# Optimization experiments

Hardware: AMD Instinct MI355X
Metric: run time of the kernel (lower is better)

Reference implementation:

```python
import jax, jax.numpy as jnp
from jax import lax
import numpy as np

# correlation hyperparams (from init_kwargs)
MAX_D = 32      # maxDisplacement
PAD = 1         # zero padding
K = 3           # patch (kernel) size
STRIDE_K = 1    # stride over output pixels
STRIDE_D = 1    # stride over displacements


def setup_inputs() -> dict:
    key = jax.random.key(0)
    k0, k1 = jax.random.split(key)
    x0 = jax.random.normal(k0, (4, 64, 256, 512), dtype=jnp.float32)
    x1 = jax.random.normal(k1, (4, 64, 256, 512), dtype=jnp.float32)
    return {"x0": x0, "x1": x1}


def _corr2d(x0, x1):
    # x0, x1: [B, C, H, W] NCHW feature maps
    B, C, H, W = x0.shape
    # zero-pad spatially; x1 gets extra width padding so all displacements are in-bounds
    x0p = jnp.pad(x0, ((0, 0), (0, 0), (PAD, PAD), (PAD, PAD)))
    x1p = jnp.pad(x1, ((0, 0), (0, 0), (PAD, PAD), (PAD + MAX_D, PAD + MAX_D)))
    Wp = W + 2 * PAD
    # width offsets into x1p for displacements d = -MAX_D .. MAX_D step STRIDE_D
    offsets = jnp.arange(0, 2 * MAX_D + 1, STRIDE_D, dtype=jnp.int32)

    def step(carry, off):
        x1s = lax.dynamic_slice_in_dim(x1p, off, Wp, axis=3)   # [B,C,Hp,Wp]
        prod = jnp.sum(x0p * x1s, axis=1)                      # channel dot -> [B,Hp,Wp]
        # KxK box-sum over the patch, stride STRIDE_K -> [B,Ho,Wo]
        s = lax.reduce_window(prod, jnp.float32(0), lax.add,
                              (1, K, K), (1, STRIDE_K, STRIDE_K), 'VALID')
        return carry, s

    _, out = lax.scan(step, None, offsets)        # [nD, B, Ho, Wo]
    out = jnp.transpose(out, (1, 0, 2, 3))        # [B, nD, Ho, Wo]
    return out / jnp.asarray(K * K * C, out.dtype)


def reference(x0, x1):
    return _corr2d(x0, x1)
```

## Files before the change

kernel.cpp:

```cpp
#include <hip/hip_runtime.h>

#define WF 512
#define HF 256
#define CF 64
#define NDTOT 65
#define DP 72

static constexpr size_t CH  = (size_t)HF * WF;
static constexpr size_t WH  = (size_t)HF * WF;
static constexpr float  INV = 1.0f / 576.0f;

typedef _Float16 f16;
typedef _Float16 f16x4 __attribute__((ext_vector_type(4)));
typedef _Float16 f16x8 __attribute__((ext_vector_type(8)));
typedef float    f32x4 __attribute__((ext_vector_type(4)));

#if __has_builtin(__builtin_amdgcn_mfma_f32_16x16x16f16)
#define MFMA16(A, B, C) __builtin_amdgcn_mfma_f32_16x16x16f16((A), (B), (C), 0, 0, 0)
#define FRAG_T f16x4
__device__ __forceinline__ f16x4 mkfrag(f16 a, f16 b, f16 c, f16 d) {
    f16x4 r; r[0] = a; r[1] = b; r[2] = c; r[3] = d; return r;
}
#else
#define MFMA16(A, B, C) __builtin_amdgcn_mfma_f32_16x16x32_f16((A), (B), (C), 0, 0, 0)
#define FRAG_T f16x8
__device__ __forceinline__ f16x8 mkfrag(f16 a, f16 b, f16 c, f16 d) {
    f16x8 r; r[0] = a; r[1] = b; r[2] = c; r[3] = d;
    r[4] = (f16)0.f; r[5] = (f16)0.f; r[6] = (f16)0.f; r[7] = (f16)0.f; return r;
}
#endif

#define GLOADF(dst, ptr, offbytes) \
    asm volatile("global_load_dword %0, %1, %2" \
                 : "=v"(dst) : "v"(offbytes), "s"(ptr))

__global__ __launch_bounds__(256) __attribute__((amdgpu_waves_per_eu(2, 4)))
void corr_gram(const float* __restrict__ x0, const float* __restrict__ x1,
               f16* __restrict__ ws) {
    const int f = blockIdx.x;
    const int tid = (f & 7) * 512 + (f >> 3);
    const int b = tid >> 10;
    const int y = (tid >> 2) & 255;
    const int sg = tid & 3;

    const int t = threadIdx.x;
    const int l = t & 63;
    const int w = t >> 6;
    const int xs = (sg * 4 + w) * 32;
    const int jb = xs - 32;

    const int n  = l & 15;
    const int kq = l >> 4;

    __shared__ f16 ebs[4][2304];

    const float* x0r = x0 + (size_t)b * CF * CH + (size_t)y * WF;
    const float* x1r = x1 + (size_t)b * CF * CH + (size_t)y * WF;

    int aB[2];
#pragma unroll
    for (int xt = 0; xt < 2; ++xt)
        aB[xt] = (4 * kq * (int)CH + xs + 16 * xt + n) * 4;
    int bB[6]; bool okj[6];
#pragma unroll
    for (int jt = 0; jt < 6; ++jt) {
        int col = jb + 16 * jt + n;
        okj[jt] = (unsigned)col < (unsigned)WF;
        col = col < 0 ? 0 : (col > 511 ? 511 : col);
        bB[jt] = (4 * kq * (int)CH + col) * 4;
    }

    f32x4 acc[10];
#pragma unroll
    for (int i = 0; i < 10; ++i) acc[i] = (f32x4)0.0f;

    float raA[8], rbA[24], raB[8], rbB[24];

#define ISSUE(kk, RA, RB) do { \
    _Pragma("unroll") for (int xt = 0; xt < 2; ++xt) \
    _Pragma("unroll") for (int i = 0; i < 4; ++i) \
        GLOADF(RA[4*xt+i], x0r, aB[xt] + (16*(kk)+i) * (int)(CH*4)); \
    _Pragma("unroll") for (int jt = 0; jt < 6; ++jt) \
    _Pragma("unroll") for (int i = 0; i < 4; ++i) \
        GLOADF(RB[4*jt+i], x1r, bB[jt] + (16*(kk)+i) * (int)(CH*4)); \
    __builtin_amdgcn_sched_barrier(0); \
} while (0)

#define TRIPLE(ai, AH, AL) do { \
    acc[ai] = MFMA16(AH, bh, acc[ai]); \
    acc[ai] = MFMA16(AH, bl, acc[ai]); \
    acc[ai] = MFMA16(AL, bh, acc[ai]); } while (0)

#define COMPUTE(RA, RB) do { \
    FRAG_T ah[2], al[2]; \
    _Pragma("unroll") for (int xt = 0; xt < 2; ++xt) { \
        const float v0 = RA[4*xt], v1 = RA[4*xt+1], v2 = RA[4*xt+2], v3 = RA[4*xt+3]; \
        const f16 h0 = (f16)v0, h1 = (f16)v1, h2 = (f16)v2, h3 = (f16)v3; \
        ah[xt] = mkfrag(h0, h1, h2, h3); \
        al[xt] = mkfrag((f16)(v0 - (float)h0), (f16)(v1 - (float)h1), \
                        (f16)(v2 - (float)h2), (f16)(v3 - (float)h3)); \
    } \
    _Pragma("unroll") for (int jt = 0; jt < 6; ++jt) { \
        float v0 = RB[4*jt], v1 = RB[4*jt+1], v2 = RB[4*jt+2], v3 = RB[4*jt+3]; \
        v0 = okj[jt] ? v0 : 0.f; v1 = okj[jt] ? v1 : 0.f; \
        v2 = okj[jt] ? v2 : 0.f; v3 = okj[jt] ? v3 : 0.f; \
        const f16 h0 = (f16)v0, h1 = (f16)v1, h2 = (f16)v2, h3 = (f16)v3; \
        const FRAG_T bh = mkfrag(h0, h1, h2, h3); \
        const FRAG_T bl = mkfrag((f16)(v0 - (float)h0), (f16)(v1 - (float)h1), \
                                 (f16)(v2 - (float)h2), (f16)(v3 - (float)h3)); \
        if (jt < 5)  TRIPLE(jt, ah[0], al[0]); \
        if (jt >= 1) TRIPLE(4 + jt, ah[1], al[1]); \
    } \
} while (0)

#define WAIT32() do { asm volatile("s_waitcnt vmcnt(32)" ::: "memory"); \
                      __builtin_amdgcn_sched_barrier(0); } while (0)
#define WAIT0()  do { asm volatile("s_waitcnt vmcnt(0)" ::: "memory"); \
                      __builtin_amdgcn_sched_barrier(0); } while (0)

    ISSUE(0, raA, rbA);
    ISSUE(1, raB, rbB);

    WAIT32();
    COMPUTE(raA, rbA);
    ISSUE(2, raA, rbA);
    WAIT32();
    COMPUTE(raB, rbB);
    ISSUE(3, raB, rbB);
    WAIT32();
    COMPUTE(raA, rbA);
    WAIT0();
    COMPUTE(raB, rbB);

#undef COMPUTE
#undef TRIPLE
#undef ISSUE
#undef WAIT32
#undef WAIT0

    f16* eb = ebs[w];
#pragma unroll
    for (int xt = 0; xt < 2; ++xt) {
#pragma unroll
        for (int p = 0; p < 5; ++p) {
            const int i = xt * 5 + p;
#pragma unroll
            for (int q = 0; q < 4; ++q) {
                const int m = kq * 4 + q;
                const int xl = xt * 16 + m;
                const int d = 16 * p + n - m;
                if ((unsigned)d < (unsigned)NDTOT)
                    eb[xl * DP + d] = (f16)acc[i][q];
            }
        }
    }
#pragma unroll
    for (int i = 0; i < 4; ++i) {
        const int idx = l + 64 * i;
        if (idx < 224) {
            const int xl = idx / 7;
            eb[xl * DP + NDTOT + (idx - 7 * xl)] = (f16)0.f;
        }
    }
    uint4* dst = (uint4*)(ws + ((size_t)(b * HF + y) * WF + xs) * DP);
    const uint4* src = (const uint4*)eb;
#pragma unroll
    for (int i = 0; i < 5; ++i) {
        const int idx = l + 64 * i;
        if (idx < 288) dst[idx] = src[idx];
    }
}

__global__ __launch_bounds__(256)
void corr_box(const f16* __restrict__ ws, float* __restrict__ out) {
    const int xt = blockIdx.x;
    const int yt = blockIdx.y;
    const int b = blockIdx.z;
    const int t = threadIdx.x;
    const int x0b = xt * 32, y0 = yt * 8;

    __shared__ f16 S[10 * 34][DP];

    for (int u = 0; u < 10; ++u) {
        const int yy = y0 - 1 + u;
        const bool yok = (unsigned)yy < (unsigned)HF;
        const f16* src = ws + ((size_t)(b * HF + yy) * WF + (x0b - 1)) * DP;
#pragma unroll
        for (int sub = 0; sub < 2; ++sub) {
            const int idx = sub * 256 + t;
            if (idx < 306) {
                const int v = idx / 9, dg = idx - v * 9;
                const int xx = x0b - 1 + v;
                f16x8 val;
#pragma unroll
                for (int jj = 0; jj < 8; ++jj) val[jj] = (f16)0.f;
                if (yok && (unsigned)xx < (unsigned)WF)
                    val = *(const f16x8*)(src + (size_t)v * DP + dg * 8);
                *(f16x8*)&S[u * 34 + v][dg * 8] = val;
            }
        }
    }
    __syncthreads();

    const int ly = t >> 5, lx = t & 31;
    const int yg = y0 + ly, xg = x0b + lx;
    float* o0 = out + (size_t)b * NDTOT * WH + (size_t)yg * WF + xg;

#pragma unroll 1
    for (int dg = 0; dg < 9; ++dg) {
        f16x8 s;
#pragma unroll
        for (int jj = 0; jj < 8; ++jj) s[jj] = (f16)0.f;
#pragma unroll
        for (int du = 0; du < 3; ++du)
#pragma unroll
            for (int dv = 0; dv < 3; ++dv)
                s += *(const f16x8*)&S[(ly + du) * 34 + (lx + dv)][dg * 8];
#pragma unroll
        for (int jj = 0; jj < 8; ++jj) {
            const int d = dg * 8 + jj;
            if (d < NDTOT) o0[(size_t)d * WH] = (float)s[jj] * INV;
        }
    }
}

__global__ void corr_naive(const float* __restrict__ x0, const float* __restrict__ x1,
                           float* __restrict__ out) {
    const size_t total = (size_t)4 * NDTOT * WH;
    size_t idx = (size_t)blockIdx.x * blockDim.x + threadIdx.x;
    if (idx >= total) return;
    const int j = (int)(idx % WF);
    const int i = (int)((idx / WF) % HF);
    const int d = (int)((idx / WH) % NDTOT);
    const int b = (int)(idx / ((size_t)NDTOT * WH));
    const int disp = d - 32;
    float s = 0.f;
    for (int u = i - 1; u <= i + 1; ++u) {
        if (u < 0 || u >= HF) continue;
        for (int v = j - 1; v <= j + 1; ++v) {
            if (v < 0 || v >= WF) continue;
            const int v1c = v + disp;
            if (v1c < 0 || v1c >= WF) continue;
            const float* p0 = x0 + (size_t)b * CF * CH + (size_t)u * WF + v;
            const float* p1 = x1 + (size_t)b * CF * CH + (size_t)u * WF + v1c;
            for (int c = 0; c < CF; ++c)
                s += p0[(size_t)c * CH] * p1[(size_t)c * CH];
        }
    }
    out[idx] = s * INV;
}

extern "C" void kernel_launch(void* const* d_in, const int* in_sizes, int n_in,
                              void* d_out, int out_size, void* d_ws, size_t ws_size,
                              hipStream_t stream) {
    const float* x0 = (const float*)d_in[0];
    const float* x1 = (const float*)d_in[1];
    float* out = (float*)d_out;

    const size_t wsNeed = (size_t)4 * HF * WF * DP * sizeof(f16);

    if (ws_size >= wsNeed) {
        f16* ws = (f16*)d_ws;
        corr_gram<<<dim3(4096), dim3(256), 0, stream>>>(x0, x1, ws);
        corr_box<<<dim3(16, 32, 4), dim3(256), 0, stream>>>(ws, out);
    } else {
        const size_t total = (size_t)4 * NDTOT * WH;
        const int blocks = (int)((total + 255) / 256);
        corr_naive<<<dim3(blocks), dim3(256), 0, stream>>>(x0, x1, out);
    }
}
```

Before: 133.1 us.

## Pipeline global loads in finer 8-register stages with rolling waitcnt

```diff
diff --git a/kernel.cpp b/kernel.cpp
--- a/kernel.cpp
+++ b/kernel.cpp
@@ -34,7 +34,7 @@
     asm volatile("global_load_dword %0, %1, %2" \
                  : "=v"(dst) : "v"(offbytes), "s"(ptr))
 
-__global__ __launch_bounds__(256) __attribute__((amdgpu_waves_per_eu(2, 4)))
+__global__ __launch_bounds__(256) __attribute__((amdgpu_waves_per_eu(3)))
 void corr_gram(const float* __restrict__ x0, const float* __restrict__ x1,
                f16* __restrict__ ws) {
     const int f = blockIdx.x;
@@ -74,69 +74,83 @@
 #pragma unroll
     for (int i = 0; i < 10; ++i) acc[i] = (f32x4)0.0f;
 
-    float raA[8], rbA[24], raB[8], rbB[24];
-
-#define ISSUE(kk, RA, RB) do { \
+    float bufs[8][8];
+    FRAG_T ah0, ah1, al0, al1;
+
+#define ISS_A(kk, B) do { \
     _Pragma("unroll") for (int xt = 0; xt < 2; ++xt) \
     _Pragma("unroll") for (int i = 0; i < 4; ++i) \
-        GLOADF(RA[4*xt+i], x0r, aB[xt] + (16*(kk)+i) * (int)(CH*4)); \
-    _Pragma("unroll") for (int jt = 0; jt < 6; ++jt) \
+        GLOADF(bufs[B][4*xt+i], x0r, aB[xt] + (16*(kk)+i) * (int)(CH*4)); \
+    __builtin_amdgcn_sched_barrier(0); \
+} while (0)
+
+#define ISS_B(kk, p, B) do { \
+    _Pragma("unroll") for (int u = 0; u < 2; ++u) \
     _Pragma("unroll") for (int i = 0; i < 4; ++i) \
-        GLOADF(RB[4*jt+i], x1r, bB[jt] + (16*(kk)+i) * (int)(CH*4)); \
+        GLOADF(bufs[B][4*u+i], x1r, bB[2*((p)-1)+u] + (16*(kk)+i) * (int)(CH*4)); \
     __builtin_amdgcn_sched_barrier(0); \
 } while (0)
+
+#define WAITN(N) do { asm volatile("s_waitcnt vmcnt(" #N ")" ::: "memory"); \
+                      __builtin_amdgcn_sched_barrier(0); } while (0)
 
 #define TRIPLE(ai, AH, AL) do { \
     acc[ai] = MFMA16(AH, bh, acc[ai]); \
     acc[ai] = MFMA16(AH, bl, acc[ai]); \
     acc[ai] = MFMA16(AL, bh, acc[ai]); } while (0)
 
-#define COMPUTE(RA, RB) do { \
-    FRAG_T ah[2], al[2]; \
-    _Pragma("unroll") for (int xt = 0; xt < 2; ++xt) { \
-        const float v0 = RA[4*xt], v1 = RA[4*xt+1], v2 = RA[4*xt+2], v3 = RA[4*xt+3]; \
-        const f16 h0 = (f16)v0, h1 = (f16)v1, h2 = (f16)v2, h3 = (f16)v3; \
-        ah[xt] = mkfrag(h0, h1, h2, h3); \
-        al[xt] = mkfrag((f16)(v0 - (float)h0), (f16)(v1 - (float)h1), \
-                        (f16)(v2 - (float)h2), (f16)(v3 - (float)h3)); \
-    } \
-    _Pragma("unroll") for (int jt = 0; jt < 6; ++jt) { \
-        float v0 = RB[4*jt], v1 = RB[4*jt+1], v2 = RB[4*jt+2], v3 = RB[4*jt+3]; \
+#define CON_A(B) do { \
+    { const float v0 = bufs[B][0], v1 = bufs[B][1], v2 = bufs[B][2], v3 = bufs[B][3]; \
+      const f16 h0 = (f16)v0, h1 = (f16)v1, h2 = (f16)v2, h3 = (f16)v3; \
+      ah0 = mkfrag(h0, h1, h2, h3); \
+      al0 = mkfrag((f16)(v0-(float)h0), (f16)(v1-(float)h1), (f16)(v2-(float)h2), (f16)(v3-(float)h3)); } \
+    { const float v0 = bufs[B][4], v1 = bufs[B][5], v2 = bufs[B][6], v3 = bufs[B][7]; \
+      const f16 h0 = (f16)v0, h1 = (f16)v1, h2 = (f16)v2, h3 = (f16)v3; \
+      ah1 = mkfrag(h0, h1, h2, h3); \
+      al1 = mkfrag((f16)(v0-(float)h0), (f16)(v1-(float)h1), (f16)(v2-(float)h2), (f16)(v3-(float)h3)); } \
+} while (0)
+
+#define CON_B(p, B) do { \
+    _Pragma("unroll") for (int u = 0; u < 2; ++u) { \
+        const int jt = 2*((p)-1) + u; \
+        float v0 = bufs[B][4*u], v1 = bufs[B][4*u+1], v2 = bufs[B][4*u+2], v3 = bufs[B][4*u+3]; \
         v0 = okj[jt] ? v0 : 0.f; v1 = okj[jt] ? v1 : 0.f; \
         v2 = okj[jt] ? v2 : 0.f; v3 = okj[jt] ? v3 : 0.f; \
         const f16 h0 = (f16)v0, h1 = (f16)v1, h2 = (f16)v2, h3 = (f16)v3; \
         const FRAG_T bh = mkfrag(h0, h1, h2, h3); \
-        const FRAG_T bl = mkfrag((f16)(v0 - (float)h0), (f16)(v1 - (float)h1), \
-                                 (f16)(v2 - (float)h2), (f16)(v3 - (float)h3)); \
-        if (jt < 5)  TRIPLE(jt, ah[0], al[0]); \
-        if (jt >= 1) TRIPLE(4 + jt, ah[1], al[1]); \
+        const FRAG_T bl = mkfrag((f16)(v0-(float)h0), (f16)(v1-(float)h1), \
+                                 (f16)(v2-(float)h2), (f16)(v3-(float)h3)); \
+        if (jt < 5)  TRIPLE(jt, ah0, al0); \
+        if (jt >= 1) TRIPLE(4 + jt, ah1, al1); \
     } \
 } while (0)
 
-#define WAIT32() do { asm volatile("s_waitcnt vmcnt(32)" ::: "memory"); \
-                      __builtin_amdgcn_sched_barrier(0); } while (0)
-#define WAIT0()  do { asm volatile("s_waitcnt vmcnt(0)" ::: "memory"); \
-                      __builtin_amdgcn_sched_barrier(0); } while (0)
-
-    ISSUE(0, raA, rbA);
-    ISSUE(1, raB, rbB);
-
-    WAIT32();
-    COMPUTE(raA, rbA);
-    ISSUE(2, raA, rbA);
-    WAIT32();
-    COMPUTE(raB, rbB);
-    ISSUE(3, raB, rbB);
-    WAIT32();
-    COMPUTE(raA, rbA);
-    WAIT0();
-    COMPUTE(raB, rbB);
-
-#undef COMPUTE
+    ISS_A(0, 0); ISS_B(0, 1, 1); ISS_B(0, 2, 2); ISS_B(0, 3, 3);
+    ISS_A(1, 4); ISS_B(1, 1, 5); ISS_B(1, 2, 6);
+
+    WAITN(48); ISS_B(1, 3, 7); CON_A(0);
+    WAITN(48); ISS_A(2, 0);    CON_B(1, 1);
+    WAITN(48); ISS_B(2, 1, 1); CON_B(2, 2);
+    WAITN(48); ISS_B(2, 2, 2); CON_B(3, 3);
+    WAITN(48); ISS_B(2, 3, 3); CON_A(4);
+    WAITN(48); ISS_A(3, 4);    CON_B(1, 5);
+    WAITN(48); ISS_B(3, 1, 5); CON_B(2, 6);
+    WAITN(48); ISS_B(3, 2, 6); CON_B(3, 7);
+    WAITN(48); ISS_B(3, 3, 7); CON_A(0);
+    WAITN(48); CON_B(1, 1);
+    WAITN(40); CON_B(2, 2);
+    WAITN(32); CON_B(3, 3);
+    WAITN(24); CON_A(4);
+    WAITN(16); CON_B(1, 5);
+    WAITN(8);  CON_B(2, 6);
+    WAITN(0);  CON_B(3, 7);
+
+#undef CON_B
+#undef CON_A
 #undef TRIPLE
-#undef ISSUE
-#undef WAIT32
-#undef WAIT0
+#undef WAITN
+#undef ISS_B
+#undef ISS_A
 
     f16* eb = ebs[w];
 #pragma unroll
```

New measurement: 133.0 us. About the same (-0.1%).
